# Optimization experiments

Measured on AMD Instinct MI355X. Metric: run time of the kernel, lower is better.

Reference implementation:

```python
import jax, jax.numpy as jnp
import numpy as np

N_HEADS = 16
MAX_SEQ_LEN = 2048


def _rotary_tables(d_k, max_seq_len):
    # Rotary.__init__: dim//4 frequencies followed by dim//4 zeros -> dim//2 entries
    freqs = (1.0 / 10000.0) ** jnp.linspace(0.0, 1.0, d_k // 4, dtype=jnp.float32)
    freqs = jnp.concatenate([freqs, jnp.zeros(d_k // 4, dtype=jnp.float32)])
    theta = jnp.arange(max_seq_len, dtype=jnp.float32)[:, None] * freqs[None, :]  # [S, d_k//2]
    return jnp.cos(theta), jnp.sin(theta)


def _apply_rotary_bug_faithful(u, cos, sin):
    # u: [B, H, T, Dk]. Original Rotary indexes cos/sin by u.size(-3) == n_heads,
    # so the rotation angle depends on the HEAD index and broadcasts over time.
    H = u.shape[1]
    c = cos[None, :H, None, :]  # [1, H, 1, Dk//2]
    s = sin[None, :H, None, :]
    u1, u2 = jnp.split(u.astype(jnp.float32), 2, axis=-1)
    y1 = u1 * c + u2 * s
    y2 = -u1 * s + u2 * c
    return jnp.concatenate([y1, y2], axis=-1).astype(u.dtype)


def setup_inputs() -> dict:
    key = jax.random.key(0)
    k1, k2, k3 = jax.random.split(key, 3)
    d_model = 2048
    B, T = 2, 2048
    x = jax.random.normal(k1, (B, T, d_model), dtype=jnp.float32)
    w_qkv = jax.random.normal(k2, (3 * d_model, d_model), dtype=jnp.float32) * (1.0 / np.sqrt(d_model))
    w_o = jax.random.normal(k3, (d_model, d_model), dtype=jnp.float32) * (1.0 / np.sqrt(d_model))
    return {"x": x, "w_qkv": w_qkv, "w_o": w_o}


def reference(x, w_qkv, w_o):
    B, T, D = x.shape
    H = N_HEADS
    dk = D // H
    cos, sin = _rotary_tables(dk, MAX_SEQ_LEN)

    # Fused QKV projection (Linear, no bias): [B,T,3D]
    qkv = jnp.einsum('btd,ed->bte', x, w_qkv)
    qkv = qkv.reshape(B, T, 3, H, dk).transpose(2, 0, 3, 1, 4)  # [3,B,H,T,dk]
    Q, K, V = qkv[0], qkv[1], qkv[2]

    Q = _apply_rotary_bug_faithful(Q, cos, sin)
    K = _apply_rotary_bug_faithful(K, cos, sin)

    # Causal scaled dot-product attention (eval mode -> dropout_p = 0)
    scale = 1.0 / np.sqrt(dk)
    scores = jnp.einsum('bhqd,bhkd->bhqk', Q, K) * scale
    causal = jnp.tril(jnp.ones((T, T), dtype=bool))
    scores = jnp.where(causal[None, None], scores, jnp.finfo(scores.dtype).min)
    attn = jax.nn.softmax(scores, axis=-1)
    out = jnp.einsum('bhqk,bhkd->bhqd', attn, V)  # [B,H,T,dk]
    out = out.transpose(0, 2, 1, 3).reshape(B, T, D)
    return jnp.einsum('btd,ed->bte', out, w_o)
```

## Files before the change

### kernel.cpp

```cpp
#include <hip/hip_runtime.h>

typedef unsigned short u16;
typedef short bf16x8 __attribute__((ext_vector_type(8)));
typedef float f32x4 __attribute__((ext_vector_type(4)));
typedef unsigned short u16x4 __attribute__((ext_vector_type(4)));

#define QK_SCALE 0.08838834764831845f

__device__ __forceinline__ u16 f2bf(float f) {
  unsigned u = __float_as_uint(f);
  u += 0x7fffu + ((u >> 16) & 1u);
  return (u16)(u >> 16);
}
__device__ __forceinline__ float bf2f(u16 h) { return __uint_as_float(((unsigned)h) << 16); }

__device__ __forceinline__ void gld_lds16(const u16* g, u16* l) {
  __builtin_amdgcn_global_load_lds(
      (const __attribute__((address_space(1))) void*)g,
      (__attribute__((address_space(3))) void*)l, 16, 0, 0);
}

__global__ void cvt_bf16_kernel(const float* __restrict__ in, u16* __restrict__ out, int n4) {
  int i = blockIdx.x * 256 + threadIdx.x;
  if (i >= n4) return;
  const float4 v = reinterpret_cast<const float4*>(in)[i];
  u16x4 o;
  o[0] = f2bf(v.x); o[1] = f2bf(v.y); o[2] = f2bf(v.z); o[3] = f2bf(v.w);
  reinterpret_cast<u16x4*>(out)[i] = o;
}

__global__ void rotw_kernel(const float* __restrict__ w, u16* __restrict__ wb) {
  const int i = blockIdx.x * 256 + threadIdx.x;
  const int k4 = i & 511;
  const int j = (i >> 9) & 63;
  const int h = (i >> 15) & 15;
  const int which = i >> 19;
  const size_t e1 = (size_t)which * 2048 + h * 128 + j;
  const size_t e2 = e1 + 64;
  const float fr = (j < 32) ? __expf(-0.2971077539f * (float)j) : 0.0f;
  float s, c;
  __sincosf((float)h * fr, &s, &c);
  const float scale = (which == 0) ? QK_SCALE : 1.0f;
  const float4 a = reinterpret_cast<const float4*>(w + e1 * 2048)[k4];
  const float4 b = reinterpret_cast<const float4*>(w + e2 * 2048)[k4];
  u16x4 o1, o2;
  o1[0] = f2bf((a.x * c + b.x * s) * scale);
  o1[1] = f2bf((a.y * c + b.y * s) * scale);
  o1[2] = f2bf((a.z * c + b.z * s) * scale);
  o1[3] = f2bf((a.w * c + b.w * s) * scale);
  o2[0] = f2bf((b.x * c - a.x * s) * scale);
  o2[1] = f2bf((b.y * c - a.y * s) * scale);
  o2[2] = f2bf((b.z * c - a.z * s) * scale);
  o2[3] = f2bf((b.w * c - a.w * s) * scale);
  reinterpret_cast<u16x4*>(wb + e1 * 2048)[k4] = o1;
  reinterpret_cast<u16x4*>(wb + e2 * 2048)[k4] = o2;
}

template<int MODE>
__global__ __launch_bounds__(512, 2) void gemm8p_kernel(
    const u16* __restrict__ A, const u16* __restrict__ Bw, int Kdim, int n_out,
    u16* __restrict__ q_out, u16* __restrict__ k_out, u16* __restrict__ v_out,
    float* __restrict__ f_out)
{
  __shared__ __align__(16) u16 As[2][256 * 64];
  __shared__ __align__(16) u16 Bs[2][256 * 64];
  const int t = threadIdx.x, lane = t & 63, w = t >> 6;
  const int wr = w >> 2, wc = w & 3;
  const int l15 = lane & 15, lhi = lane >> 4;
  const int flat = blockIdx.y * 16 + blockIdx.x;
  const int swz = (flat & 7) * 48 + (flat >> 3);
  const int m0 = (swz & 15) << 8, n0 = (swz >> 4) << 8;
  const int NT = Kdim >> 6;

  const int srow = w * 8 + (lane >> 3);
  const int gchunk = (lane & 7) ^ (srow & 7);
  const size_t gcol = (size_t)gchunk * 8;

  auto stageA2 = [&](int buf, int kt2, int half) {
    const size_t kb = (size_t)kt2 * 64 + gcol;
#pragma unroll
    for (int i = 0; i < 2; ++i) {
      const int ro = half * 128 + i * 64;
      gld_lds16(A + (size_t)(m0 + srow + ro) * Kdim + kb, &As[buf][(w * 8 + ro) * 64]);
    }
  };
  auto stageB4 = [&](int buf, int kt2) {
    const size_t kb = (size_t)kt2 * 64 + gcol;
#pragma unroll
    for (int ro = 0; ro < 256; ro += 64)
      gld_lds16(Bw + (size_t)(n0 + srow + ro) * Kdim + kb, &Bs[buf][(w * 8 + ro) * 64]);
  };

  const int arow0 = (wr * 128 + l15) * 64;
  const int brow0 = (wc * 64 + l15) * 64;
  const int koff0 = ((0 + lhi) ^ (l15 & 7)) * 8;
  const int koff1 = ((4 + lhi) ^ (l15 & 7)) * 8;

  f32x4 acc[8][4];
#pragma unroll
  for (int m = 0; m < 8; ++m)
#pragma unroll
    for (int n = 0; n < 4; ++n)
#pragma unroll
      for (int i = 0; i < 4; ++i) acc[m][n][i] = 0.0f;

  stageA2(0, 0, 0); stageA2(0, 0, 1);
  stageB4(0, 0);
  if (NT > 1) { stageA2(1, 1, 0); stageA2(1, 1, 1); }
  asm volatile("s_waitcnt vmcnt(4)" ::: "memory");
  __builtin_amdgcn_s_barrier();

  for (int kt = 0; kt < NT; ++kt) {
    const int cur = kt & 1;
    const u16* __restrict__ Ac = &As[cur][0];
    const u16* __restrict__ Bc = &Bs[cur][0];
    bf16x8 aK1[4], a2K1[4], b0[4], b1[4];
    {
      bf16x8 aK0[4];
#pragma unroll
      for (int m = 0; m < 4; ++m) {
        aK0[m] = *reinterpret_cast<const bf16x8*>(Ac + arow0 + m * 1024 + koff0);
        aK1[m] = *reinterpret_cast<const bf16x8*>(Ac + arow0 + m * 1024 + koff1);
      }
#pragma unroll
      for (int n = 0; n < 4; ++n)
        b0[n] = *reinterpret_cast<const bf16x8*>(Bc + brow0 + n * 1024 + koff0);
      if (kt + 1 < NT) stageB4(cur ^ 1, kt + 1);
      __builtin_amdgcn_s_barrier();
      asm volatile("s_waitcnt lgkmcnt(0)" ::: "memory");
      __builtin_amdgcn_s_setprio(1);
#pragma unroll
      for (int m = 0; m < 4; ++m)
#pragma unroll
        for (int n = 0; n < 4; ++n)
          acc[m][n] = __builtin_amdgcn_mfma_f32_16x16x32_bf16(aK0[m], b0[n], acc[m][n], 0, 0, 0);
      __builtin_amdgcn_s_setprio(0);
      __builtin_amdgcn_s_barrier();
    }
    {
      bf16x8 a2K0[4];
#pragma unroll
      for (int m = 0; m < 4; ++m) {
        a2K0[m] = *reinterpret_cast<const bf16x8*>(Ac + arow0 + (m + 4) * 1024 + koff0);
        a2K1[m] = *reinterpret_cast<const bf16x8*>(Ac + arow0 + (m + 4) * 1024 + koff1);
      }
#pragma unroll
      for (int n = 0; n < 4; ++n)
        b1[n] = *reinterpret_cast<const bf16x8*>(Bc + brow0 + n * 1024 + koff1);
      __builtin_amdgcn_s_barrier();
      asm volatile("s_waitcnt lgkmcnt(0)" ::: "memory");
      __builtin_amdgcn_s_setprio(1);
#pragma unroll
      for (int m = 0; m < 4; ++m)
#pragma unroll
        for (int n = 0; n < 4; ++n)
          acc[m + 4][n] = __builtin_amdgcn_mfma_f32_16x16x32_bf16(a2K0[m], b0[n], acc[m + 4][n], 0, 0, 0);
      __builtin_amdgcn_s_setprio(0);
      __builtin_amdgcn_s_barrier();
    }
    if (kt + 2 < NT) stageA2(cur, kt + 2, 0);
    __builtin_amdgcn_s_barrier();
    __builtin_amdgcn_s_setprio(1);
#pragma unroll
    for (int m = 0; m < 4; ++m)
#pragma unroll
      for (int n = 0; n < 4; ++n)
        acc[m][n] = __builtin_amdgcn_mfma_f32_16x16x32_bf16(aK1[m], b1[n], acc[m][n], 0, 0, 0);
    __builtin_amdgcn_s_setprio(0);
    __builtin_amdgcn_s_barrier();
    if (kt + 2 < NT) stageA2(cur, kt + 2, 1);
    __builtin_amdgcn_s_barrier();
    __builtin_amdgcn_s_setprio(1);
#pragma unroll
    for (int m = 0; m < 4; ++m)
#pragma unroll
      for (int n = 0; n < 4; ++n)
        acc[m + 4][n] = __builtin_amdgcn_mfma_f32_16x16x32_bf16(a2K1[m], b1[n], acc[m + 4][n], 0, 0, 0);
    __builtin_amdgcn_s_setprio(0);
    if (kt < NT - 2) { asm volatile("s_waitcnt vmcnt(4)" ::: "memory"); }
    else             { asm volatile("s_waitcnt vmcnt(0)" ::: "memory"); }
    __builtin_amdgcn_s_barrier();
  }

  const int rb = wr * 128 + lhi * 4;
  const int cb = wc * 64 + l15;
  if (MODE == 0) {
#pragma unroll
    for (int n = 0; n < 4; ++n) {
      const int e = n0 + cb + n * 16;
      const int which = e >> 11;
      const int h = (e >> 7) & 15;
      const int d = e & 127;
#pragma unroll
      for (int m = 0; m < 8; ++m)
#pragma unroll
        for (int r = 0; r < 4; ++r) {
          const int bt = m0 + rb + m * 16 + r;
          const int bb = bt >> 11, tt = bt & 2047;
          const float val = acc[m][n][r];
          if (which == 2) {
            v_out[((size_t)(bb * 16 + h) * 128 + d) * 2048 + tt] = f2bf(val);
          } else {
            u16* dst = (which == 0) ? q_out : k_out;
            dst[((size_t)(bb * 16 + h) * 2048 + tt) * 128 + d] = f2bf(val);
          }
        }
    }
  } else {
#pragma unroll
    for (int m = 0; m < 8; ++m)
#pragma unroll
      for (int r = 0; r < 4; ++r) {
        const int row = m0 + rb + m * 16 + r;
#pragma unroll
        for (int n = 0; n < 4; ++n)
          f_out[(size_t)row * n_out + n0 + cb + n * 16] = acc[m][n][r];
      }
  }
}

__global__ __launch_bounds__(256) void gemm_bt_kernel(
    const u16* __restrict__ A, const u16* __restrict__ Bw, int Kdim, int n_out,
    float* __restrict__ f_out)
{
  __shared__ __align__(16) u16 Asl[128 * 32];
  __shared__ __align__(16) u16 Bsl[128 * 32];
  const int t = threadIdx.x;
  const int lane = t & 63;
  const int w = t >> 6;
  const int wr = w >> 1, wc = w & 1;
  const int flat = blockIdx.y * 32 + blockIdx.x;
  const int swz = (flat & 7) * 64 + (flat >> 3);
  const int m0 = (swz & 31) << 7, n0 = (swz >> 5) << 7;

  f32x4 acc[4][4];
#pragma unroll
  for (int m = 0; m < 4; ++m)
#pragma unroll
    for (int n = 0; n < 4; ++n)
#pragma unroll
      for (int i = 0; i < 4; ++i) acc[m][n][i] = 0.0f;

  const int ob0 = w * 1024 + lane * 16;
  const int row0 = ob0 >> 6;
  const int cole0 = (ob0 & 63) >> 1;
  const u16* gA0 = A + (size_t)(m0 + row0) * Kdim + cole0;
  const u16* gA1 = gA0 + (size_t)64 * Kdim;
  const u16* gB0 = Bw + (size_t)(n0 + row0) * Kdim + cole0;
  const u16* gB1 = gB0 + (size_t)64 * Kdim;
  u16* lA = Asl + w * 512;
  u16* lB = Bsl + w * 512;

  const int l15 = lane & 15;
  const int kb = (lane >> 4) * 8;

  for (int k0 = 0; k0 < Kdim; k0 += 32) {
    __syncthreads();
    gld_lds16(gA0, lA);
    gld_lds16(gA1, lA + 2048);
    gld_lds16(gB0, lB);
    gld_lds16(gB1, lB + 2048);
    gA0 += 32; gA1 += 32; gB0 += 32; gB1 += 32;
    __syncthreads();
    bf16x8 a[4], b[4];
#pragma unroll
    for (int m = 0; m < 4; ++m)
      a[m] = *reinterpret_cast<const bf16x8*>(Asl + (wr * 64 + m * 16 + l15) * 32 + kb);
#pragma unroll
    for (int n = 0; n < 4; ++n)
      b[n] = *reinterpret_cast<const bf16x8*>(Bsl + (wc * 64 + n * 16 + l15) * 32 + kb);
#pragma unroll
    for (int m = 0; m < 4; ++m)
#pragma unroll
      for (int n = 0; n < 4; ++n)
        acc[m][n] = __builtin_amdgcn_mfma_f32_16x16x32_bf16(a[m], b[n], acc[m][n], 0, 0, 0);
  }

  const int rb = wr * 64 + ((lane >> 4) << 2);
  const int cbs = wc * 64 + l15;
#pragma unroll
  for (int m = 0; m < 4; ++m)
#pragma unroll
    for (int r = 0; r < 4; ++r) {
      const int row = m0 + rb + m * 16 + r;
#pragma unroll
      for (int n = 0; n < 4; ++n)
        f_out[(size_t)row * n_out + n0 + cbs + n * 16] = acc[m][n][r];
    }
}

__global__ __launch_bounds__(256) void attn_kernel(
    const u16* __restrict__ Q, const u16* __restrict__ K,
    const u16* __restrict__ Vt, u16* __restrict__ O)
{
  __shared__ __align__(16) u16 k_lds[2][64 * 128];
  __shared__ __align__(16) u16 v_lds[2][128 * 64];
  __shared__ __align__(16) u16 p_lds[4][1024];
  const int t = threadIdx.x, lane = t & 63, w = t >> 6;
  const int flat = blockIdx.y * 16 + blockIdx.x;
  const int swz = (flat & 7) * 64 + (flat >> 3);
  const int bx = swz & 15;
  const int bh = swz >> 4;
  const int l15 = lane & 15, lhi = lane >> 4;
  const size_t qkb = (size_t)bh * (2048 * 128);
  const u16* Kg = K + qkb;
  const u16* Vg = Vt + (size_t)bh * (size_t)(128 * 2048);
  char* pw = (char*)(&p_lds[w][0]);
  const int bb = bh >> 4, h = bh & 15;
  const int kxor = (l15 & 7) << 4;

  auto stage = [&](int buf, int k0) {
#pragma unroll
    for (int ii = 0; ii < 4; ++ii) {
      const int i = w * 4 + ii;
      const int krow = i * 4 + lhi;
      gld_lds16(Kg + (size_t)(k0 + krow) * 128 + (size_t)((l15 ^ (krow & 7)) * 8),
                &k_lds[buf][i * 512]);
    }
#pragma unroll
    for (int ii = 0; ii < 4; ++ii) {
      const int i = w * 4 + ii;
      const int vrow = i * 8 + (lane >> 3);
      gld_lds16(Vg + (size_t)vrow * 2048 + k0 + (size_t)(((lane & 7) ^ (vrow & 7)) * 8),
                &v_lds[buf][i * 512]);
    }
  };

  for (int half = 0; half < 2; ++half) {
    const int qt = half ? (31 - bx) : bx;
    const int q0 = qt * 64 + w * 16;
    bf16x8 aq[4];
    {
      const u16* qp = Q + qkb + (size_t)(q0 + l15) * 128 + lhi * 8;
#pragma unroll
      for (int ks = 0; ks < 4; ++ks) aq[ks] = *reinterpret_cast<const bf16x8*>(qp + ks * 32);
    }
    f32x4 o[8];
#pragma unroll
    for (int dt = 0; dt < 8; ++dt)
#pragma unroll
      for (int i = 0; i < 4; ++i) o[dt][i] = 0.0f;
    float mrow[4] = {-1e30f, -1e30f, -1e30f, -1e30f};
    float lrow[4] = {0.f, 0.f, 0.f, 0.f};
    const int rbase = q0 + (lhi << 2);
    const int ktmax = qt;

    __syncthreads();
    stage(0, 0);
    int cur = 0;
    for (int kt = 0; kt <= ktmax; ++kt) {
      __syncthreads();
      if (kt < ktmax) stage(cur ^ 1, (kt + 1) * 64);

      const char* kbb = (const char*)(&k_lds[cur][0]);
      f32x4 s4[4];
#pragma unroll
      for (int nt = 0; nt < 4; ++nt)
#pragma unroll
        for (int i = 0; i < 4; ++i) s4[nt][i] = 0.0f;
#pragma unroll
      for (int nt = 0; nt < 4; ++nt) {
        const int krow = nt * 16 + l15;
#pragma unroll
        for (int ks = 0; ks < 4; ++ks) {
          const bf16x8 bk = *reinterpret_cast<const bf16x8*>(
              kbb + krow * 256 + ((ks * 64 + lhi * 16) ^ kxor));
          s4[nt] = __builtin_amdgcn_mfma_f32_16x16x32_bf16(aq[ks], bk, s4[nt], 0, 0, 0);
        }
      }
      if (kt == ktmax) {
#pragma unroll
        for (int nt = 0; nt < 4; ++nt) {
          const int col = kt * 64 + nt * 16 + l15;
#pragma unroll
          for (int r = 0; r < 4; ++r)
            if (col > rbase + r) s4[nt][r] = -1e30f;
        }
      }
      float alpha[4];
#pragma unroll
      for (int r = 0; r < 4; ++r) {
        float mx = fmaxf(fmaxf(s4[0][r], s4[1][r]), fmaxf(s4[2][r], s4[3][r]));
        mx = fmaxf(mx, __shfl_xor(mx, 1));
        mx = fmaxf(mx, __shfl_xor(mx, 2));
        mx = fmaxf(mx, __shfl_xor(mx, 4));
        mx = fmaxf(mx, __shfl_xor(mx, 8));
        const float mn = fmaxf(mrow[r], mx);
        alpha[r] = __expf(mrow[r] - mn);
        mrow[r] = mn;
      }
      float ps[4] = {0.f, 0.f, 0.f, 0.f};
#pragma unroll
      for (int nt = 0; nt < 4; ++nt)
#pragma unroll
        for (int r = 0; r < 4; ++r) {
          const float p = __expf(s4[nt][r] - mrow[r]);
          ps[r] += p;
          const int prow = (lhi << 2) + r;
          const int cbyte = (nt * 16 + l15) * 2;
          *(u16*)(pw + prow * 128 + (cbyte ^ ((prow & 7) << 4))) = f2bf(p);
        }
#pragma unroll
      for (int r = 0; r < 4; ++r) {
        float rs = ps[r];
        rs += __shfl_xor(rs, 1);
        rs += __shfl_xor(rs, 2);
        rs += __shfl_xor(rs, 4);
        rs += __shfl_xor(rs, 8);
        lrow[r] = lrow[r] * alpha[r] + rs;
#pragma unroll
        for (int dt = 0; dt < 8; ++dt) o[dt][r] *= alpha[r];
      }
      const char* vbb = (const char*)(&v_lds[cur][0]);
#pragma unroll
      for (int ks2 = 0; ks2 < 2; ++ks2) {
        const bf16x8 ap = *reinterpret_cast<const bf16x8*>(
            pw + l15 * 128 + ((ks2 * 64 + (lhi << 4)) ^ kxor));
#pragma unroll
        for (int dt = 0; dt < 8; ++dt) {
          const int vrow = dt * 16 + l15;
          const bf16x8 bv = *reinterpret_cast<const bf16x8*>(
              vbb + vrow * 128 + ((ks2 * 64 + lhi * 16) ^ kxor));
          o[dt] = __builtin_amdgcn_mfma_f32_16x16x32_bf16(ap, bv, o[dt], 0, 0, 0);
        }
      }
      cur ^= 1;
    }
#pragma unroll
    for (int r = 0; r < 4; ++r) {
      const float inv = 1.0f / lrow[r];
      const int row = rbase + r;
      u16* op = O + (size_t)(bb * 2048 + row) * 2048 + h * 128 + l15;
#pragma unroll
      for (int dt = 0; dt < 8; ++dt) op[dt * 16] = f2bf(o[dt][r] * inv);
    }
  }
}

extern "C" void kernel_launch(void* const* d_in, const int* in_sizes, int n_in,
                              void* d_out, int out_size, void* d_ws, size_t ws_size,
                              hipStream_t stream) {
  const float* x = (const float*)d_in[0];
  const float* wqkv = (const float*)d_in[1];
  const float* wo = (const float*)d_in[2];
  float* out = (float*)d_out;
  u16* ws = (u16*)d_ws;

  u16* xb = ws;
  u16* wqkvb = xb + 8388608;
  u16* wob = wqkvb + 12582912;
  u16* Qb = wob + 4194304;
  u16* Kb = Qb + 8388608;
  u16* Vtb = Kb + 8388608;
  u16* attn = xb;

  cvt_bf16_kernel<<<8192, 256, 0, stream>>>(x, xb, 2097152);
  rotw_kernel<<<4096, 256, 0, stream>>>(wqkv, wqkvb);
  cvt_bf16_kernel<<<4096, 256, 0, stream>>>(wqkv + (size_t)4096 * 2048,
                                            wqkvb + (size_t)4096 * 2048, 1048576);
  cvt_bf16_kernel<<<4096, 256, 0, stream>>>(wo, wob, 1048576);

  gemm8p_kernel<0><<<dim3(16, 24), 512, 0, stream>>>(xb, wqkvb, 2048, 0, Qb, Kb, Vtb, nullptr);

  attn_kernel<<<dim3(16, 32), 256, 0, stream>>>(Qb, Kb, Vtb, attn);

  gemm_bt_kernel<<<dim3(32, 16), 256, 0, stream>>>(attn, wob, 2048, 2048, out);
}
```

Before: 346.7 us.

## Write V row-major from QKV GEMM and transpose it in a separate kernel

```diff
diff --git a/kernel.cpp b/kernel.cpp
--- a/kernel.cpp
+++ b/kernel.cpp
@@ -67,9 +67,7 @@
   const int t = threadIdx.x, lane = t & 63, w = t >> 6;
   const int wr = w >> 2, wc = w & 3;
   const int l15 = lane & 15, lhi = lane >> 4;
-  const int flat = blockIdx.y * 16 + blockIdx.x;
-  const int swz = (flat & 7) * 48 + (flat >> 3);
-  const int m0 = (swz & 15) << 8, n0 = (swz >> 4) << 8;
+  const int m0 = blockIdx.x * 256, n0 = blockIdx.y * 256;
   const int NT = Kdim >> 6;
 
   const int srow = w * 8 + (lane >> 3);
@@ -191,19 +189,14 @@
       const int which = e >> 11;
       const int h = (e >> 7) & 15;
       const int d = e & 127;
+      u16* dst = (which == 0) ? q_out : (which == 1) ? k_out : v_out;
 #pragma unroll
       for (int m = 0; m < 8; ++m)
 #pragma unroll
         for (int r = 0; r < 4; ++r) {
           const int bt = m0 + rb + m * 16 + r;
           const int bb = bt >> 11, tt = bt & 2047;
-          const float val = acc[m][n][r];
-          if (which == 2) {
-            v_out[((size_t)(bb * 16 + h) * 128 + d) * 2048 + tt] = f2bf(val);
-          } else {
-            u16* dst = (which == 0) ? q_out : k_out;
-            dst[((size_t)(bb * 16 + h) * 2048 + tt) * 128 + d] = f2bf(val);
-          }
+          dst[((size_t)(bb * 16 + h) * 2048 + tt) * 128 + d] = f2bf(acc[m][n][r]);
         }
     }
   } else {
@@ -229,9 +222,7 @@
   const int lane = t & 63;
   const int w = t >> 6;
   const int wr = w >> 1, wc = w & 1;
-  const int flat = blockIdx.y * 32 + blockIdx.x;
-  const int swz = (flat & 7) * 64 + (flat >> 3);
-  const int m0 = (swz & 31) << 7, n0 = (swz >> 5) << 7;
+  const int m0 = blockIdx.x * 128, n0 = blockIdx.y * 128;
 
   f32x4 acc[4][4];
 #pragma unroll
@@ -289,6 +280,34 @@
     }
 }
 
+__global__ void transpose_v_kernel(const u16* __restrict__ V, u16* __restrict__ Vt) {
+  __shared__ u16 tile[64][65];
+  const int d0 = blockIdx.x * 64;
+  const int t0 = blockIdx.y * 64;
+  const int bh = blockIdx.z;
+  const u16* src = V + (size_t)bh * (2048 * 128);
+  u16* dst = Vt + (size_t)bh * (128 * 2048);
+  const int tid = threadIdx.x;
+  const int c4 = (tid & 15) * 4;
+  const int r0 = tid >> 4;
+#pragma unroll
+  for (int p = 0; p < 4; ++p) {
+    const int row = r0 + p * 16;
+    const u16x4 v = *reinterpret_cast<const u16x4*>(src + (size_t)(t0 + row) * 128 + d0 + c4);
+    tile[row][c4] = v[0]; tile[row][c4 + 1] = v[1];
+    tile[row][c4 + 2] = v[2]; tile[row][c4 + 3] = v[3];
+  }
+  __syncthreads();
+#pragma unroll
+  for (int p = 0; p < 4; ++p) {
+    const int dr = r0 + p * 16;
+    u16x4 ov;
+    ov[0] = tile[c4][dr]; ov[1] = tile[c4 + 1][dr];
+    ov[2] = tile[c4 + 2][dr]; ov[3] = tile[c4 + 3][dr];
+    *reinterpret_cast<u16x4*>(dst + (size_t)(d0 + dr) * 2048 + t0 + c4) = ov;
+  }
+}
+
 __global__ __launch_bounds__(256) void attn_kernel(
     const u16* __restrict__ Q, const u16* __restrict__ K,
     const u16* __restrict__ Vt, u16* __restrict__ O)
@@ -297,10 +316,8 @@
   __shared__ __align__(16) u16 v_lds[2][128 * 64];
   __shared__ __align__(16) u16 p_lds[4][1024];
   const int t = threadIdx.x, lane = t & 63, w = t >> 6;
-  const int flat = blockIdx.y * 16 + blockIdx.x;
-  const int swz = (flat & 7) * 64 + (flat >> 3);
-  const int bx = swz & 15;
-  const int bh = swz >> 4;
+  const int bh = blockIdx.y;
+  const int bx = blockIdx.x;
   const int l15 = lane & 15, lhi = lane >> 4;
   const size_t qkb = (size_t)bh * (2048 * 128);
   const u16* Kg = K + qkb;
@@ -451,7 +468,8 @@
   u16* wob = wqkvb + 12582912;
   u16* Qb = wob + 4194304;
   u16* Kb = Qb + 8388608;
-  u16* Vtb = Kb + 8388608;
+  u16* Vb = Kb + 8388608;
+  u16* Vtb = wqkvb;
   u16* attn = xb;
 
   cvt_bf16_kernel<<<8192, 256, 0, stream>>>(x, xb, 2097152);
@@ -460,7 +478,9 @@
                                             wqkvb + (size_t)4096 * 2048, 1048576);
   cvt_bf16_kernel<<<4096, 256, 0, stream>>>(wo, wob, 1048576);
 
-  gemm8p_kernel<0><<<dim3(16, 24), 512, 0, stream>>>(xb, wqkvb, 2048, 0, Qb, Kb, Vtb, nullptr);
+  gemm8p_kernel<0><<<dim3(16, 24), 512, 0, stream>>>(xb, wqkvb, 2048, 0, Qb, Kb, Vb, nullptr);
+
+  transpose_v_kernel<<<dim3(2, 32, 32), 256, 0, stream>>>(Vb, Vtb);
 
   attn_kernel<<<dim3(16, 32), 256, 0, stream>>>(Qb, Kb, Vtb, attn);
 
```

After: 311.6 us, median of 2. -10.1%, faster.
